# Performance work log

Hardware: AMD Instinct MI355X
Metric: run time of the kernel (lower is better)

## Reference

```python
import jax, jax.numpy as jnp
import numpy as np

N = 16384          # num nodes (128 graphs x 128 turbines)
E = 262144         # edges before self loops
TURBINE_NUM = 128
D_IN = 512         # input_dim (= 2*hidden_dim1)
H1 = 256           # hidden_dim1
H2 = 256           # hidden_dim2
NEG_SLOPE = 0.2    # PyG GATConv default leaky relu slope


def _glorot(key, shape, fan_in):
    return jax.random.normal(key, shape, dtype=jnp.float32) / np.sqrt(fan_in)


def setup_inputs() -> dict:
    key = jax.random.key(0)
    ks = jax.random.split(key, 12)
    x = jax.random.normal(ks[0], (N, H2), dtype=jnp.float32)
    adj = jax.random.randint(ks[1], (2, E), 0, N, dtype=jnp.int64)
    # fc: Linear(hidden_dim2 -> hidden_dim1); stored as [in, out]
    W_fc = _glorot(ks[2], (H2, H1), H2)
    b_fc = jnp.zeros((H1,), dtype=jnp.float32)
    # gat1: GATConv(H1 -> H1, heads=2, concat)
    W1 = _glorot(ks[3], (H1, 2 * H1), H1)
    a1_src = _glorot(ks[4], (2, H1), H1)
    a1_dst = _glorot(ks[5], (2, H1), H1)
    b1 = jnp.zeros((2 * H1,), dtype=jnp.float32)
    # gat2: GATConv(D_IN -> D_IN, heads=1, concat)
    W2 = _glorot(ks[6], (D_IN, D_IN), D_IN)
    a2_src = _glorot(ks[7], (1, D_IN), D_IN)
    a2_dst = _glorot(ks[8], (1, D_IN), D_IN)
    b2 = jnp.zeros((D_IN,), dtype=jnp.float32)
    return dict(x=x, adj=adj, W_fc=W_fc, b_fc=b_fc, W1=W1, a1_src=a1_src,
                a1_dst=a1_dst, b1=b1, W2=W2, a2_src=a2_src, a2_dst=a2_dst, b2=b2)


def gat_conv(x, src, dst, W, a_src, a_dst, bias, heads, out_ch):
    """PyG GATConv (eval mode, self loops already in src/dst)."""
    n = x.shape[0]
    h = (x @ W).reshape(n, heads, out_ch)                 # [N,H,C]
    al_s = jnp.einsum('nhc,hc->nh', h, a_src)             # [N,H]
    al_d = jnp.einsum('nhc,hc->nh', h, a_dst)
    e = jax.nn.leaky_relu(al_s[src] + al_d[dst], NEG_SLOPE)  # [E,H]
    # segment softmax over incoming edges per destination node
    e_max = jax.ops.segment_max(e, dst, num_segments=n)
    e_exp = jnp.exp(e - e_max[dst])
    denom = jax.ops.segment_sum(e_exp, dst, num_segments=n)
    alpha = e_exp / (denom[dst] + 1e-16)                  # [E,H]
    msg = h[src] * alpha[:, :, None]                      # [E,H,C]
    out = jax.ops.segment_sum(msg, dst, num_segments=n)   # [N,H,C]
    return out.reshape(n, heads * out_ch) + bias


def reference(x, adj, W_fc, b_fc, W1, a1_src, a1_dst, b1, W2, a2_src, a2_dst, b2):
    # add self loops (PyG GATConv default)
    loops = jnp.arange(N, dtype=adj.dtype)
    src = jnp.concatenate([adj[0], loops])
    dst = jnp.concatenate([adj[1], loops])
    h = jax.nn.relu(x @ W_fc + b_fc)                      # fc + ReLU
    h = gat_conv(h, src, dst, W1, a1_src, a1_dst, b1, heads=2, out_ch=H1)
    h = jax.nn.relu(h)
    h = gat_conv(h, src, dst, W2, a2_src, a2_dst, b2, heads=1, out_ch=D_IN)
    y = jax.nn.relu(h)
    return y.reshape(-1, TURBINE_NUM, y.shape[1])         # [128,128,512]
```

## Files before the change

### kernel.cpp

```cpp
#include <hip/hip_runtime.h>

#define N_NODES 16384
#define N_EDGES 262144
#define E_TOT   (N_EDGES + N_NODES)
#define NEG_SLOPE 0.2f

typedef __attribute__((ext_vector_type(8))) short short8;
typedef __attribute__((ext_vector_type(4))) float floatx4;
typedef __attribute__((ext_vector_type(4))) int intx4;

__device__ __forceinline__ float bf2f(ushort u) {
    return __uint_as_float(((unsigned)u) << 16);
}
__device__ __forceinline__ ushort f2bf(float f) {
    unsigned u = __float_as_uint(f);
    u += 0x7fffu + ((u >> 16) & 1u);
    return (ushort)(u >> 16);
}
__device__ __forceinline__ float leaky(float x) {
    return x > 0.f ? x : NEG_SLOPE * x;
}

#define PREP_CAST   524288
#define PREP_T1     (PREP_CAST + 65536)
#define PREP_T2     (PREP_T1 + 131072)
#define PREP_Z      (PREP_T2 + 262144)
#define PREP_ZA     (PREP_Z + 4096)
#define PREP_V      (PREP_ZA + 24576)
#define PREP_TOT    (PREP_V + 131072)

__global__ __launch_bounds__(256) void k_prep(const float* __restrict__ x,
                                              ushort* __restrict__ xb,
                                              const float* __restrict__ Wfc,
                                              ushort* __restrict__ WfcT,
                                              const float* __restrict__ W1,
                                              ushort* __restrict__ W1T,
                                              const float* __restrict__ W2,
                                              ushort* __restrict__ W2T,
                                              int* __restrict__ counts,
                                              int* __restrict__ alzero,
                                              const float* __restrict__ a1s,
                                              const float* __restrict__ a1d,
                                              const float* __restrict__ a2s,
                                              const float* __restrict__ a2d,
                                              float* __restrict__ v1s,
                                              float* __restrict__ v1d,
                                              float* __restrict__ v2s,
                                              float* __restrict__ v2d) {
    int idx = blockIdx.x * 256 + threadIdx.x;
    if (idx < PREP_CAST) {
        floatx4 v0 = *(const floatx4*)(x + (size_t)idx * 8);
        floatx4 v1 = *(const floatx4*)(x + (size_t)idx * 8 + 4);
        short8 r;
        r[0] = (short)f2bf(v0[0]); r[1] = (short)f2bf(v0[1]);
        r[2] = (short)f2bf(v0[2]); r[3] = (short)f2bf(v0[3]);
        r[4] = (short)f2bf(v1[0]); r[5] = (short)f2bf(v1[1]);
        r[6] = (short)f2bf(v1[2]); r[7] = (short)f2bf(v1[3]);
        *(short8*)(xb + (size_t)idx * 8) = r;
    } else if (idx < PREP_T1) {
        int t = idx - PREP_CAST;
        int k = t >> 8, n = t & 255;
        WfcT[n * 256 + k] = f2bf(Wfc[t]);
    } else if (idx < PREP_T2) {
        int t = idx - PREP_T1;
        int k = t >> 9, n = t & 511;
        W1T[n * 256 + k] = f2bf(W1[t]);
    } else if (idx < PREP_Z) {
        int t = idx - PREP_T2;
        int k = t >> 9, n = t & 511;
        W2T[n * 512 + k] = f2bf(W2[t]);
    } else if (idx < PREP_ZA) {
        int t = idx - PREP_Z;
        *(intx4*)(counts + t * 4) = (intx4){0, 0, 0, 0};
    } else if (idx < PREP_V) {
        int t = idx - PREP_ZA;
        *(intx4*)(alzero + t * 4) = (intx4){0, 0, 0, 0};
    } else if (idx < PREP_TOT) {
        int t = idx - PREP_V;
        int w = t >> 6, lane = t & 63;
        int grp = w >> 9;
        int o = w & 511;
        float sum;
        if (grp < 2) {
            const float* a = grp ? a1d : a1s;
            int h = o >> 8, k = o & 255;
            const float* wr = W1 + (size_t)k * 512 + h * 256;
            const float* ar = a + h * 256;
            floatx4 wv = *(const floatx4*)(wr + lane * 4);
            floatx4 av = *(const floatx4*)(ar + lane * 4);
            sum = wv[0]*av[0] + wv[1]*av[1] + wv[2]*av[2] + wv[3]*av[3];
        } else {
            const float* a = (grp == 2) ? a2s : a2d;
            const float* wr = W2 + (size_t)o * 512;
            floatx4 w0 = *(const floatx4*)(wr + lane * 8);
            floatx4 w1 = *(const floatx4*)(wr + lane * 8 + 4);
            floatx4 a0 = *(const floatx4*)(a + lane * 8);
            floatx4 a1 = *(const floatx4*)(a + lane * 8 + 4);
            sum = w0[0]*a0[0] + w0[1]*a0[1] + w0[2]*a0[2] + w0[3]*a0[3]
                + w1[0]*a1[0] + w1[1]*a1[1] + w1[2]*a1[2] + w1[3]*a1[3];
        }
#pragma unroll
        for (int msk = 1; msk < 64; msk <<= 1) sum += __shfl_xor(sum, msk, 64);
        if (lane == 0) {
            float* dst = (grp == 0) ? v1s : (grp == 1) ? v1d
                        : (grp == 2) ? v2s : v2d;
            dst[o] = sum;
        }
    }
}

__global__ __launch_bounds__(256) void k_hist(const int* __restrict__ adj,
                                              int* __restrict__ counts) {
    int e = blockIdx.x * 256 + threadIdx.x;
    if (e < E_TOT) {
        int d = (e < N_EDGES) ? adj[N_EDGES + e] : (e - N_EDGES);
        atomicAdd(&counts[d], 1);
    }
}

__global__ __launch_bounds__(1024) void k_scan(const int* __restrict__ counts,
                                               int* __restrict__ offs,
                                               int* __restrict__ cursor) {
    __shared__ int wsum[16];
    int t = threadIdx.x, lane = t & 63, w = t >> 6;
    int local[16];
    int tot = 0;
#pragma unroll
    for (int i = 0; i < 16; i++) {
        local[i] = tot;
        tot += counts[t * 16 + i];
    }
    int incl = tot;
#pragma unroll
    for (int d = 1; d < 64; d <<= 1) {
        int v = __shfl_up(incl, d, 64);
        if (lane >= d) incl += v;
    }
    if (lane == 63) wsum[w] = incl;
    __syncthreads();
    if (w == 0) {
        int v = (lane < 16) ? wsum[lane] : 0;
#pragma unroll
        for (int d = 1; d < 16; d <<= 1) {
            int u = __shfl_up(v, d, 64);
            if (lane >= d) v += u;
        }
        if (lane < 16) wsum[lane] = v;
    }
    __syncthreads();
    int base = ((w == 0) ? 0 : wsum[w - 1]) + incl - tot;
#pragma unroll
    for (int i = 0; i < 16; i++) {
        int o = base + local[i];
        offs[t * 16 + i] = o;
        cursor[t * 16 + i] = o;
    }
    if (t == 1023) offs[N_NODES] = wsum[15];
}

__global__ __launch_bounds__(256) void k_scatter(const int* __restrict__ adj,
                                                 int* __restrict__ cursor,
                                                 int* __restrict__ esrc) {
    int e = blockIdx.x * 256 + threadIdx.x;
    if (e < E_TOT) {
        int s, d;
        if (e < N_EDGES) { s = adj[e]; d = adj[N_EDGES + e]; }
        else             { s = e - N_EDGES; d = s; }
        int pos = atomicAdd(&cursor[d], 1);
        esrc[pos] = s;
    }
}

#define GM 128
#define GN 128
#define GK 64
#define LDK2 72

__global__ __launch_bounds__(256) void gemm128(const ushort* __restrict__ A,
                                               int lda, int agrp,
                                               const ushort* __restrict__ BT,
                                               const float* __restrict__ bias,
                                               ushort* __restrict__ C,
                                               float* __restrict__ Cf,
                                               int M, int Nc, int K, int relu,
                                               const float* __restrict__ vs,
                                               const float* __restrict__ vd,
                                               float* __restrict__ als,
                                               float* __restrict__ ald,
                                               int heads) {
    __shared__ ushort As[GM * LDK2];
    __shared__ ushort Bs[GN * LDK2];
    int tid = threadIdx.x, wave = tid >> 6, lane = tid & 63;
    int quad = lane >> 4, l16 = lane & 15;
    int bm = blockIdx.x * GM, bn = blockIdx.y * GN;
    int wm = (wave & 1) * 64, wn = (wave >> 1) * 64;
    int abase = (bn >> 8) * agrp;

    floatx4 acc[4][4];
#pragma unroll
    for (int mi = 0; mi < 4; mi++)
#pragma unroll
        for (int ni = 0; ni < 4; ni++)
            acc[mi][ni] = (floatx4){0.f, 0.f, 0.f, 0.f};

    int srow[4], scol[4];
#pragma unroll
    for (int t = 0; t < 4; t++) {
        int ci = tid + 256 * t;
        srow[t] = ci >> 3;
        scol[t] = (ci & 7) * 8;
    }

    short8 av[4], bv[4];
#pragma unroll
    for (int t = 0; t < 4; t++) {
        av[t] = *(const short8*)(A + (size_t)(bm + srow[t]) * lda + abase + scol[t]);
        bv[t] = *(const short8*)(BT + (size_t)(bn + srow[t]) * K + scol[t]);
    }

    for (int kb = 0; kb < K; kb += GK) {
        if (kb) {
            asm volatile("s_waitcnt lgkmcnt(0)" ::: "memory");
            __builtin_amdgcn_sched_barrier(0);
            __builtin_amdgcn_s_barrier();
            __builtin_amdgcn_sched_barrier(0);
        }
#pragma unroll
        for (int t = 0; t < 4; t++) {
            *(short8*)&As[srow[t] * LDK2 + scol[t]] = av[t];
            *(short8*)&Bs[srow[t] * LDK2 + scol[t]] = bv[t];
        }
        asm volatile("s_waitcnt lgkmcnt(0)" ::: "memory");
        __builtin_amdgcn_sched_barrier(0);
        __builtin_amdgcn_s_barrier();
        __builtin_amdgcn_sched_barrier(0);

        if (kb + GK < K) {
#pragma unroll
            for (int t = 0; t < 4; t++) {
                av[t] = *(const short8*)(A + (size_t)(bm + srow[t]) * lda + abase + kb + GK + scol[t]);
                bv[t] = *(const short8*)(BT + (size_t)(bn + srow[t]) * K + kb + GK + scol[t]);
            }
            __builtin_amdgcn_sched_barrier(0);
        }

#pragma unroll
        for (int kk = 0; kk < GK; kk += 32) {
            short8 af[4], bf[4];
#pragma unroll
            for (int mi = 0; mi < 4; mi++)
                af[mi] = *(const short8*)&As[(wm + mi * 16 + l16) * LDK2 + kk + quad * 8];
#pragma unroll
            for (int ni = 0; ni < 4; ni++)
                bf[ni] = *(const short8*)&Bs[(wn + ni * 16 + l16) * LDK2 + kk + quad * 8];
#pragma unroll
            for (int mi = 0; mi < 4; mi++)
#pragma unroll
                for (int ni = 0; ni < 4; ni++)
                    acc[mi][ni] = __builtin_amdgcn_mfma_f32_16x16x32_bf16(
                        af[mi], bf[ni], acc[mi][ni], 0, 0, 0);
        }
    }

#pragma unroll
    for (int mi = 0; mi < 4; mi++) {
        int row = bm + wm + mi * 16 + quad * 4;
#pragma unroll
        for (int ni = 0; ni < 4; ni++) {
            int col = bn + wn + ni * 16 + l16;
            float bv2 = bias ? bias[col] : 0.f;
#pragma unroll
            for (int i = 0; i < 4; i++) {
                float v = acc[mi][ni][i] + bv2;
                if (relu) v = fmaxf(v, 0.f);
                acc[mi][ni][i] = v;
                if (Cf) Cf[(size_t)(row + i) * Nc + col] = v;
                else    C[(size_t)(row + i) * Nc + col] = f2bf(v);
            }
        }
    }

    if (als) {
        if (heads == 2) {
            float s0[4], s1[4], d0[4], d1[4];
#pragma unroll
            for (int ni = 0; ni < 4; ni++) {
                int col = bn + wn + ni * 16 + l16;
                s0[ni] = vs[col];  s1[ni] = vs[256 + col];
                d0[ni] = vd[col];  d1[ni] = vd[256 + col];
            }
#pragma unroll
            for (int mi = 0; mi < 4; mi++) {
#pragma unroll
                for (int i = 0; i < 4; i++) {
                    float aS0 = 0.f, aS1 = 0.f, aD0 = 0.f, aD1 = 0.f;
#pragma unroll
                    for (int ni = 0; ni < 4; ni++) {
                        float vv = acc[mi][ni][i];
                        aS0 += vv * s0[ni]; aS1 += vv * s1[ni];
                        aD0 += vv * d0[ni]; aD1 += vv * d1[ni];
                    }
#pragma unroll
                    for (int msk = 1; msk < 16; msk <<= 1) {
                        aS0 += __shfl_xor(aS0, msk, 64);
                        aS1 += __shfl_xor(aS1, msk, 64);
                        aD0 += __shfl_xor(aD0, msk, 64);
                        aD1 += __shfl_xor(aD1, msk, 64);
                    }
                    if (l16 == 0) {
                        int row = bm + wm + mi * 16 + quad * 4 + i;
                        atomicAdd(&als[row * 2],     aS0);
                        atomicAdd(&als[row * 2 + 1], aS1);
                        atomicAdd(&ald[row * 2],     aD0);
                        atomicAdd(&ald[row * 2 + 1], aD1);
                    }
                }
            }
        } else {
            float aS[4], aD[4];
#pragma unroll
            for (int ni = 0; ni < 4; ni++) {
                int col = bn + wn + ni * 16 + l16;
                aS[ni] = vs[col];
                aD[ni] = vd[col];
            }
#pragma unroll
            for (int mi = 0; mi < 4; mi++) {
#pragma unroll
                for (int i = 0; i < 4; i++) {
                    float dS = 0.f, dD = 0.f;
#pragma unroll
                    for (int ni = 0; ni < 4; ni++) {
                        dS += acc[mi][ni][i] * aS[ni];
                        dD += acc[mi][ni][i] * aD[ni];
                    }
#pragma unroll
                    for (int msk = 1; msk < 16; msk <<= 1) {
                        dS += __shfl_xor(dS, msk, 64);
                        dD += __shfl_xor(dD, msk, 64);
                    }
                    if (l16 == 0) {
                        int row = bm + wm + mi * 16 + quad * 4 + i;
                        atomicAdd(&als[row], dS);
                        atomicAdd(&ald[row], dD);
                    }
                }
            }
        }
    }
}

__global__ __launch_bounds__(256) void k_agg(const ushort* __restrict__ h,
                                             const float* __restrict__ als,
                                             const float* __restrict__ ald,
                                             const int* __restrict__ offs,
                                             const int* __restrict__ esrc,
                                             ushort* __restrict__ outb,
                                             int heads) {
    int wave = threadIdx.x >> 6, lane = threadIdx.x & 63;
    int n = blockIdx.x * 4 + wave;
    int base = offs[n];
    int deg  = offs[n + 1] - base;

    int myhead = (heads == 2) ? (lane >> 5) : 0;
    int cs = (heads == 2) ? ((lane & 31) * 8) : (lane * 8);
    int stride = (heads == 2) ? 256 : 512;

    float aldh0 = ald[n * heads];
    float aldh1 = (heads == 2) ? ald[n * heads + 1] : 0.f;
    const ushort* hc = h + cs;

    float acc[8];
#pragma unroll
    for (int q = 0; q < 8; q++) acc[q] = 0.f;
    float ws0 = 0.f, ws1 = 0.f;

    for (int cb = 0; cb < deg; cb += 64) {
        int i = cb + lane;
        int sv = 0;
        float w0 = 0.f, w1 = 0.f;
        if (i < deg) {
            sv = esrc[base + i];
            w0 = __expf(leaky(als[sv * heads] + aldh0));
            if (heads == 2) w1 = __expf(leaky(als[sv * 2 + 1] + aldh1));
            ws0 += w0; ws1 += w1;
        }
        int cnt = min(64, deg - cb);
        int j = 0;
        for (; j + 4 <= cnt; j += 4) {
            int sj0 = __shfl(sv, j, 64);
            int sj1 = __shfl(sv, j + 1, 64);
            int sj2 = __shfl(sv, j + 2, 64);
            int sj3 = __shfl(sv, j + 3, 64);
            float a00 = __shfl(w0, j, 64),     a01 = __shfl(w1, j, 64);
            float a10 = __shfl(w0, j + 1, 64), a11 = __shfl(w1, j + 1, 64);
            float a20 = __shfl(w0, j + 2, 64), a21 = __shfl(w1, j + 2, 64);
            float a30 = __shfl(w0, j + 3, 64), a31 = __shfl(w1, j + 3, 64);
            float al0 = myhead ? a01 : a00;
            float al1 = myhead ? a11 : a10;
            float al2 = myhead ? a21 : a20;
            float al3 = myhead ? a31 : a30;
            short8 h0v = *(const short8*)(hc + (size_t)sj0 * stride);
            short8 h1v = *(const short8*)(hc + (size_t)sj1 * stride);
            short8 h2v = *(const short8*)(hc + (size_t)sj2 * stride);
            short8 h3v = *(const short8*)(hc + (size_t)sj3 * stride);
#pragma unroll
            for (int q = 0; q < 8; q++) {
                acc[q] += al0 * bf2f((ushort)h0v[q]);
                acc[q] += al1 * bf2f((ushort)h1v[q]);
                acc[q] += al2 * bf2f((ushort)h2v[q]);
                acc[q] += al3 * bf2f((ushort)h3v[q]);
            }
        }
        for (; j < cnt; j++) {
            int s = __shfl(sv, j, 64);
            float a0 = __shfl(w0, j, 64), a1 = __shfl(w1, j, 64);
            float al = myhead ? a1 : a0;
            short8 hv = *(const short8*)(hc + (size_t)s * stride);
#pragma unroll
            for (int q = 0; q < 8; q++) acc[q] += al * bf2f((ushort)hv[q]);
        }
    }

#pragma unroll
    for (int msk = 1; msk < 64; msk <<= 1) {
        ws0 += __shfl_xor(ws0, msk, 64);
        ws1 += __shfl_xor(ws1, msk, 64);
    }
    float inv = 1.f / ((myhead ? ws1 : ws0) + 1e-16f);

    short8 r;
#pragma unroll
    for (int q = 0; q < 8; q++) r[q] = (short)f2bf(acc[q] * inv);
    *(short8*)(outb + (size_t)n * 512 + lane * 8) = r;
}

extern "C" void kernel_launch(void* const* d_in, const int* in_sizes, int n_in,
                              void* d_out, int out_size, void* d_ws, size_t ws_size,
                              hipStream_t stream) {
    const float* x   = (const float*)d_in[0];
    const int*   adj = (const int*)d_in[1];
    const float* Wfc = (const float*)d_in[2];
    const float* bfc = (const float*)d_in[3];
    const float* W1  = (const float*)d_in[4];
    const float* a1s = (const float*)d_in[5];
    const float* a1d = (const float*)d_in[6];
    const float* b1  = (const float*)d_in[7];
    const float* W2  = (const float*)d_in[8];
    const float* a2s = (const float*)d_in[9];
    const float* a2d = (const float*)d_in[10];
    const float* b2  = (const float*)d_in[11];
    float* out = (float*)d_out;

    char* ws = (char*)d_ws;
    size_t off = 0;
    auto alloc = [&](size_t bytes) -> void* {
        void* p = ws + off;
        off += (bytes + 255) & ~(size_t)255;
        return p;
    };
    ushort* xb   = (ushort*)alloc((size_t)N_NODES * 256 * 2);
    ushort* h0b  = (ushort*)alloc((size_t)N_NODES * 256 * 2);
    ushort* hub  = (ushort*)alloc((size_t)N_NODES * 512 * 2);
    ushort* g1b  = (ushort*)alloc((size_t)N_NODES * 512 * 2);
    int* counts  = (int*)alloc(N_NODES * 4);
    int* offs    = (int*)alloc((N_NODES + 1) * 4);
    int* cursor  = (int*)alloc(N_NODES * 4);
    int* esrc    = (int*)alloc(E_TOT * 4);
    ushort* WfcT = (ushort*)alloc(256 * 256 * 2);
    ushort* W1T  = (ushort*)alloc(512 * 256 * 2);
    ushort* W2T  = (ushort*)alloc(512 * 512 * 2);
    float* als1  = (float*)alloc(N_NODES * 2 * 4);
    float* ald1  = (float*)alloc(N_NODES * 2 * 4);
    float* als2  = (float*)alloc(N_NODES * 4);
    float* ald2  = (float*)alloc(N_NODES * 4);
    float* v1s   = (float*)alloc(512 * 4);
    float* v1d   = (float*)alloc(512 * 4);
    float* v2s   = (float*)alloc(512 * 4);
    float* v2d   = (float*)alloc(512 * 4);

    k_prep<<<PREP_TOT / 256, 256, 0, stream>>>(x, xb, Wfc, WfcT, W1, W1T, W2, W2T,
                                               counts, (int*)als1,
                                               a1s, a1d, a2s, a2d,
                                               v1s, v1d, v2s, v2d);

    k_hist<<<(E_TOT + 255) / 256, 256, 0, stream>>>(adj, counts);
    k_scan<<<1, 1024, 0, stream>>>(counts, offs, cursor);
    k_scatter<<<(E_TOT + 255) / 256, 256, 0, stream>>>(adj, cursor, esrc);

    gemm128<<<dim3(N_NODES / GM, 256 / GN), 256, 0, stream>>>(
        xb, 256, 0, WfcT, bfc, h0b, nullptr, N_NODES, 256, 256, 1,
        v1s, v1d, als1, ald1, 2);
    k_agg<<<N_NODES / 4, 256, 0, stream>>>(h0b, als1, ald1, offs, esrc, hub, 2);

    gemm128<<<dim3(N_NODES / GM, 512 / GN), 256, 0, stream>>>(
        hub, 512, 256, W1T, b1, g1b, nullptr, N_NODES, 512, 256, 1,
        v2s, v2d, als2, ald2, 1);
    k_agg<<<N_NODES / 4, 256, 0, stream>>>(g1b, als2, ald2, offs, esrc, hub, 1);

    gemm128<<<dim3(N_NODES / GM, 512 / GN), 256, 0, stream>>>(
        hub, 512, 0, W2T, b2, nullptr, out, N_NODES, 512, 512, 1,
        nullptr, nullptr, nullptr, nullptr, 0);
}
```

Baseline: 242.8 us.

## Split GAT aggregation across column groups with edge-parallel lane slots

Rewrites the aggregation kernel so each block handles a 64-column slice of a node. The eight lane groups in a wave each process different edges, and partial sums are reduced with cross-lane shuffles. For the two-head layer, both heads come from one shared h row (the first layer's output gets reused by the weights), so one load feeds two accumulators. This adds more blocks and more parallel gathers per node to hide memory latency. The cost is recomputing the edge weights once per column group and an extra shuffle reduction. The scan kernel also vectorizes its count loads.

Measured after the change: 302.1 us. +24.4%, slower.

```diff
diff --git a/kernel.cpp b/kernel.cpp
--- a/kernel.cpp
+++ b/kernel.cpp
@@ -123,12 +123,15 @@
                                                int* __restrict__ cursor) {
     __shared__ int wsum[16];
     int t = threadIdx.x, lane = t & 63, w = t >> 6;
+    intx4 c[4];
+#pragma unroll
+    for (int i = 0; i < 4; i++) c[i] = *(const intx4*)(counts + t * 16 + i * 4);
     int local[16];
     int tot = 0;
 #pragma unroll
     for (int i = 0; i < 16; i++) {
         local[i] = tot;
-        tot += counts[t * 16 + i];
+        tot += c[i >> 2][i & 3];
     }
     int incl = tot;
 #pragma unroll
@@ -350,89 +353,81 @@
     }
 }
 
-__global__ __launch_bounds__(256) void k_agg(const ushort* __restrict__ h,
-                                             const float* __restrict__ als,
-                                             const float* __restrict__ ald,
-                                             const int* __restrict__ offs,
-                                             const int* __restrict__ esrc,
-                                             ushort* __restrict__ outb,
-                                             int heads) {
+__global__ __launch_bounds__(256) void k_aggs(const ushort* __restrict__ h,
+                                              const float* __restrict__ als,
+                                              const float* __restrict__ ald,
+                                              const int* __restrict__ offs,
+                                              const int* __restrict__ esrc,
+                                              ushort* __restrict__ outb,
+                                              int heads, int cgs) {
     int wave = threadIdx.x >> 6, lane = threadIdx.x & 63;
-    int n = blockIdx.x * 4 + wave;
+    int cg   = blockIdx.x % cgs;
+    int n    = (blockIdx.x / cgs) * 4 + wave;
+    int slot = lane >> 3;
+    int coff = (lane & 7) * 8;
+    int stride = (heads == 2) ? 256 : 512;
+
     int base = offs[n];
     int deg  = offs[n + 1] - base;
 
-    int myhead = (heads == 2) ? (lane >> 5) : 0;
-    int cs = (heads == 2) ? ((lane & 31) * 8) : (lane * 8);
-    int stride = (heads == 2) ? 256 : 512;
-
     float aldh0 = ald[n * heads];
     float aldh1 = (heads == 2) ? ald[n * heads + 1] : 0.f;
-    const ushort* hc = h + cs;
-
-    float acc[8];
-#pragma unroll
-    for (int q = 0; q < 8; q++) acc[q] = 0.f;
+    const ushort* hc = h + cg * 64 + coff;
+
+    float acc0[8], acc1[8];
+#pragma unroll
+    for (int q = 0; q < 8; q++) { acc0[q] = 0.f; acc1[q] = 0.f; }
     float ws0 = 0.f, ws1 = 0.f;
 
-    for (int cb = 0; cb < deg; cb += 64) {
-        int i = cb + lane;
-        int sv = 0;
-        float w0 = 0.f, w1 = 0.f;
+    for (int cb = 0; cb < deg; cb += 8) {
+        int i = cb + slot;
         if (i < deg) {
-            sv = esrc[base + i];
-            w0 = __expf(leaky(als[sv * heads] + aldh0));
-            if (heads == 2) w1 = __expf(leaky(als[sv * 2 + 1] + aldh1));
-            ws0 += w0; ws1 += w1;
-        }
-        int cnt = min(64, deg - cb);
-        int j = 0;
-        for (; j + 4 <= cnt; j += 4) {
-            int sj0 = __shfl(sv, j, 64);
-            int sj1 = __shfl(sv, j + 1, 64);
-            int sj2 = __shfl(sv, j + 2, 64);
-            int sj3 = __shfl(sv, j + 3, 64);
-            float a00 = __shfl(w0, j, 64),     a01 = __shfl(w1, j, 64);
-            float a10 = __shfl(w0, j + 1, 64), a11 = __shfl(w1, j + 1, 64);
-            float a20 = __shfl(w0, j + 2, 64), a21 = __shfl(w1, j + 2, 64);
-            float a30 = __shfl(w0, j + 3, 64), a31 = __shfl(w1, j + 3, 64);
-            float al0 = myhead ? a01 : a00;
-            float al1 = myhead ? a11 : a10;
-            float al2 = myhead ? a21 : a20;
-            float al3 = myhead ? a31 : a30;
-            short8 h0v = *(const short8*)(hc + (size_t)sj0 * stride);
-            short8 h1v = *(const short8*)(hc + (size_t)sj1 * stride);
-            short8 h2v = *(const short8*)(hc + (size_t)sj2 * stride);
-            short8 h3v = *(const short8*)(hc + (size_t)sj3 * stride);
-#pragma unroll
-            for (int q = 0; q < 8; q++) {
-                acc[q] += al0 * bf2f((ushort)h0v[q]);
-                acc[q] += al1 * bf2f((ushort)h1v[q]);
-                acc[q] += al2 * bf2f((ushort)h2v[q]);
-                acc[q] += al3 * bf2f((ushort)h3v[q]);
-            }
-        }
-        for (; j < cnt; j++) {
-            int s = __shfl(sv, j, 64);
-            float a0 = __shfl(w0, j, 64), a1 = __shfl(w1, j, 64);
-            float al = myhead ? a1 : a0;
+            int s = esrc[base + i];
+            float w0 = __expf(leaky(als[s * heads] + aldh0));
+            ws0 += w0;
             short8 hv = *(const short8*)(hc + (size_t)s * stride);
-#pragma unroll
-            for (int q = 0; q < 8; q++) acc[q] += al * bf2f((ushort)hv[q]);
-        }
-    }
-
-#pragma unroll
-    for (int msk = 1; msk < 64; msk <<= 1) {
+            if (heads == 2) {
+                float w1 = __expf(leaky(als[s * 2 + 1] + aldh1));
+                ws1 += w1;
+#pragma unroll
+                for (int q = 0; q < 8; q++) {
+                    float f = bf2f((ushort)hv[q]);
+                    acc0[q] += w0 * f;
+                    acc1[q] += w1 * f;
+                }
+            } else {
+#pragma unroll
+                for (int q = 0; q < 8; q++)
+                    acc0[q] += w0 * bf2f((ushort)hv[q]);
+            }
+        }
+    }
+
+#pragma unroll
+    for (int msk = 8; msk < 64; msk <<= 1) {
         ws0 += __shfl_xor(ws0, msk, 64);
         ws1 += __shfl_xor(ws1, msk, 64);
-    }
-    float inv = 1.f / ((myhead ? ws1 : ws0) + 1e-16f);
-
-    short8 r;
-#pragma unroll
-    for (int q = 0; q < 8; q++) r[q] = (short)f2bf(acc[q] * inv);
-    *(short8*)(outb + (size_t)n * 512 + lane * 8) = r;
+#pragma unroll
+        for (int q = 0; q < 8; q++) {
+            acc0[q] += __shfl_xor(acc0[q], msk, 64);
+            acc1[q] += __shfl_xor(acc1[q], msk, 64);
+        }
+    }
+    float inv0 = 1.f / (ws0 + 1e-16f);
+    float inv1 = 1.f / (ws1 + 1e-16f);
+
+    if (slot == 0) {
+        short8 r;
+#pragma unroll
+        for (int q = 0; q < 8; q++) r[q] = (short)f2bf(acc0[q] * inv0);
+        *(short8*)(outb + (size_t)n * 512 + cg * 64 + coff) = r;
+    }
+    if (heads == 2 && slot == 1) {
+        short8 r;
+#pragma unroll
+        for (int q = 0; q < 8; q++) r[q] = (short)f2bf(acc1[q] * inv1);
+        *(short8*)(outb + (size_t)n * 512 + 256 + cg * 64 + coff) = r;
+    }
 }
 
 extern "C" void kernel_launch(void* const* d_in, const int* in_sizes, int n_in,
@@ -491,12 +486,14 @@
     gemm128<<<dim3(N_NODES / GM, 256 / GN), 256, 0, stream>>>(
         xb, 256, 0, WfcT, bfc, h0b, nullptr, N_NODES, 256, 256, 1,
         v1s, v1d, als1, ald1, 2);
-    k_agg<<<N_NODES / 4, 256, 0, stream>>>(h0b, als1, ald1, offs, esrc, hub, 2);
+    k_aggs<<<(N_NODES / 4) * 4, 256, 0, stream>>>(h0b, als1, ald1, offs, esrc,
+                                                  hub, 2, 4);
 
     gemm128<<<dim3(N_NODES / GM, 512 / GN), 256, 0, stream>>>(
         hub, 512, 256, W1T, b1, g1b, nullptr, N_NODES, 512, 256, 1,
         v2s, v2d, als2, ald2, 1);
-    k_agg<<<N_NODES / 4, 256, 0, stream>>>(g1b, als2, ald2, offs, esrc, hub, 1);
+    k_aggs<<<(N_NODES / 4) * 8, 256, 0, stream>>>(g1b, als2, ald2, offs, esrc,
+                                                  hub, 1, 8);
 
     gemm128<<<dim3(N_NODES / GM, 512 / GN), 256, 0, stream>>>(
         hub, 512, 0, W2T, b2, nullptr, out, N_NODES, 512, 512, 1,
```
